# Performance work log

Hardware: AMD Instinct MI355X
Metric: run time of the kernel (lower is better)

## Reference

```python
import jax, jax.numpy as jnp
import numpy as np

N_FZ, N_KEZ, N_TINT, N_ALPHA = 60, 20, 30, 200
NORB, NTIMES = 2000, 1000


def setup_inputs() -> dict:
    key = jax.random.key(0)
    k1, k2, k3, k4 = jax.random.split(key, 4)
    # log-spaced coordinate axes (as built in __init__ from fZs / alphas)
    log_fZs = jnp.linspace(-11.0, -9.0, N_FZ, dtype=jnp.float32)
    log_alphas = jnp.linspace(-2.0, 0.0, N_ALPHA, dtype=jnp.float32)
    alphas = 10.0 ** log_alphas
    kEZs = jnp.linspace(0.5, 10.0, N_KEZ, dtype=jnp.float32)  # sorted for searchsorted
    # grid already in stored layout (n_fZ, n_kEZ, n_tint, n_alpha)
    grid = 20.0 + 5.0 * jax.random.uniform(k1, (N_FZ, N_KEZ, N_TINT, N_ALPHA), dtype=jnp.float32)
    # angular separations, mostly inside [alphas[0], alphas[-1]] with some outside
    alpha = 10.0 ** jax.random.uniform(k2, (NORB, NTIMES), minval=-2.2, maxval=0.1, dtype=jnp.float32)
    dMag = 20.0 + 5.0 * jax.random.uniform(k3, (NORB, NTIMES), dtype=jnp.float32)
    fZ_vals = 10.0 ** jax.random.uniform(k4, (NTIMES,), minval=-11.0, maxval=-9.0, dtype=jnp.float32)
    kEZ_val = jnp.asarray(3.0, dtype=jnp.float32)
    return dict(alpha=alpha, dMag=dMag, fZ_vals=fZ_vals, kEZ_val=kEZ_val,
                grid=grid, kEZs=kEZs, alphas=alphas, log_fZs=log_fZs, log_alphas=log_alphas)


def reference(alpha, dMag, fZ_vals, kEZ_val, grid, kEZs, alphas, log_fZs, log_alphas):
    """Faithful translation of dMag0Grid._pdet_alpha_dMag.

    alpha, dMag : (norb, ntimes); fZ_vals : (ntimes,); kEZ_val : scalar.
    grid : (n_fZ, n_kEZ, n_tint, n_alpha).  Returns pdet : (ntimes, n_tint).
    """
    n_fZ = grid.shape[0]
    n_alpha = grid.shape[-1]
    inv_log_fZ_step = 1.0 / (log_fZs[1] - log_fZs[0])
    inv_log_alpha_step = 1.0 / (log_alphas[1] - log_alphas[0])

    geom_mask = (alpha >= alphas[0]) & (alpha <= alphas[-1])  # (norb, ntimes)

    # log-binned fZ index, per time
    fZ_ind = (jnp.log10(fZ_vals) - log_fZs[0]) * inv_log_fZ_step
    fZ0 = jnp.clip(jnp.floor(fZ_ind).astype(jnp.int32) + 1, 0, n_fZ - 2)  # (ntimes,)

    # log-binned alpha index, per (orbit, time)
    a_ind = (jnp.log10(alpha) - log_alphas[0]) * inv_log_alpha_step
    a0 = jnp.clip(a_ind.astype(jnp.int32), 0, n_alpha - 1)  # (norb, ntimes)
    dalpha = (a_ind - a0).astype(grid.dtype)

    kEZ_ind = jnp.searchsorted(kEZs, kEZ_val, side='right') - 1  # scalar

    # dynamic_slice clamps start so the size-2 window stays in bounds
    a0s = jnp.minimum(a0, n_alpha - 2)
    fZb = jnp.broadcast_to(fZ0[None, :], a0.shape)  # (norb, ntimes)

    sub = grid[:, kEZ_ind]          # (n_fZ, n_tint, n_alpha)
    g0 = sub[fZb, :, a0s]           # (norb, ntimes, n_tint) gather
    g1 = sub[fZb, :, a0s + 1]
    dim = g0 + dalpha[..., None] * (g1 - g0)  # linear interp in log-alpha

    det_mask = geom_mask[..., None] & jnp.signbit(dMag[..., None] - dim)
    pdet = det_mask.mean(axis=0)    # (ntimes, n_tint)
    return pdet
```

## Files before the change

### kernel.cpp

```cpp
#include <hip/hip_runtime.h>
#include <math.h>

#define N_FZ    60
#define N_KEZ   20
#define N_TINT  30
#define N_ALPHA 200
#define NORB    2000
#define NTIMES  1000
#define BLOCK   256

__global__ __launch_bounds__(256) void prep_kernel(
    const float* __restrict__ alpha,
    const float* __restrict__ dMag,
    const float* __restrict__ alphas,
    const float* __restrict__ log_alphas,
    float2* __restrict__ xd)
{
    __shared__ float2 tile[32][33];

    const float la0    = log_alphas[0];
    const float inv_la = 1.0f / (log_alphas[1] - la0);
    const float alo    = alphas[0];
    const float ahi    = alphas[N_ALPHA - 1];

    const int t0 = blockIdx.x * 32;
    const int o0 = blockIdx.y * 32;
    const int tx = threadIdx.x, ty = threadIdx.y;

    #pragma unroll
    for (int r = 0; r < 4; ++r) {
        int orb = o0 + ty + 8 * r;
        int t   = t0 + tx;
        float2 v = make_float2(0.0f, __builtin_inff());
        if (orb < NORB && t < NTIMES) {
            float a  = alpha[(size_t)orb * NTIMES + t];
            float dm = dMag [(size_t)orb * NTIMES + t];
            bool geom = (a >= alo) && (a <= ahi);
            float x = (log10f(a) - la0) * inv_la;
            v = make_float2(x, geom ? dm : __builtin_inff());
        }
        tile[ty + 8 * r][tx] = v;
    }
    __syncthreads();
    #pragma unroll
    for (int r = 0; r < 4; ++r) {
        int tt  = ty + 8 * r;
        int t   = t0 + tt;
        int orb = o0 + tx;
        if (orb < NORB && t < NTIMES)
            xd[(size_t)t * NORB + orb] = tile[tx][tt];
    }
}

__global__ __launch_bounds__(BLOCK) void pdet2_kernel(
    const float2* __restrict__ xd,
    const float* __restrict__ fZ_vals,
    const float* __restrict__ kEZ_val,
    const float* __restrict__ grid,
    const float* __restrict__ kEZs,
    const float* __restrict__ log_fZs,
    float* __restrict__ out)
{
    __shared__ float2 pairs[N_TINT * N_ALPHA];
    __shared__ int    wsum[BLOCK / 64][N_TINT];

    const int t   = blockIdx.x;
    const int tid = threadIdx.x;

    const float lf0    = log_fZs[0];
    const float lfstep = log_fZs[1] - lf0;
    double fZ_ind = (log10((double)fZ_vals[t]) - (double)lf0) * (1.0 / (double)lfstep);
    int fZ0 = (int)floor(fZ_ind) + 1;
    fZ0 = min(max(fZ0, 0), N_FZ - 2);

    const float kv = kEZ_val[0];
    int kidx = -1;
    #pragma unroll
    for (int i = 0; i < N_KEZ; ++i) kidx += (kEZs[i] <= kv) ? 1 : 0;
    if (kidx < 0) kidx += N_KEZ;

    const float* src = grid + ((size_t)fZ0 * N_KEZ + kidx) * (N_TINT * N_ALPHA);
    const float4* src4 = (const float4*)src;
    for (int j = tid; j < (N_TINT * N_ALPHA) / 4; j += BLOCK) {
        float4 v  = src4[j];
        float nxt = src[4 * j + 4];
        pairs[4 * j + 0] = make_float2(v.x, v.y);
        pairs[4 * j + 1] = make_float2(v.y, v.z);
        pairs[4 * j + 2] = make_float2(v.z, v.w);
        pairs[4 * j + 3] = make_float2(v.w, nxt);
    }
    __syncthreads();

    int cnt[N_TINT];
    #pragma unroll
    for (int k = 0; k < N_TINT; ++k) cnt[k] = 0;

    const float4* row = (const float4*)(xd + (size_t)t * NORB);
    for (int i = tid; i < NORB / 2; i += BLOCK) {
        float4 v = row[i];
        float xA = v.x, dmA = v.y;
        float xB = v.z, dmB = v.w;

        int   a0A = min(max((int)xA, 0), N_ALPHA - 1);
        float dalA = xA - (float)a0A;
        int   aA  = min(a0A, N_ALPHA - 2);

        int   a0B = min(max((int)xB, 0), N_ALPHA - 1);
        float dalB = xB - (float)a0B;
        int   aB  = min(a0B, N_ALPHA - 2);

        #pragma unroll
        for (int k = 0; k < N_TINT; ++k) {
            float2 pA = pairs[k * N_ALPHA + aA];
            float2 pB = pairs[k * N_ALPHA + aB];
            float dimA = pA.x + dalA * (pA.y - pA.x);
            float dimB = pB.x + dalB * (pB.y - pB.x);
            cnt[k] += (dmA < dimA) ? 1 : 0;
            cnt[k] += (dmB < dimB) ? 1 : 0;
        }
    }

    const int lane = tid & 63;
    const int wid  = tid >> 6;
    #pragma unroll
    for (int k = 0; k < N_TINT; ++k) {
        int c = cnt[k];
        c += __shfl_xor(c, 32, 64);
        c += __shfl_xor(c, 16, 64);
        c += __shfl_xor(c,  8, 64);
        c += __shfl_xor(c,  4, 64);
        c += __shfl_xor(c,  2, 64);
        c += __shfl_xor(c,  1, 64);
        if (lane == 0) wsum[wid][k] = c;
    }
    __syncthreads();

    if (tid < N_TINT) {
        int tot = wsum[0][tid] + wsum[1][tid] + wsum[2][tid] + wsum[3][tid];
        out[(size_t)t * N_TINT + tid] = (float)tot / (float)NORB;
    }
}

__global__ __launch_bounds__(BLOCK) void pdet_kernel(
    const float* __restrict__ alpha, const float* __restrict__ dMag,
    const float* __restrict__ fZ_vals, const float* __restrict__ kEZ_val,
    const float* __restrict__ grid, const float* __restrict__ kEZs,
    const float* __restrict__ alphas, const float* __restrict__ log_fZs,
    const float* __restrict__ log_alphas, float* __restrict__ out)
{
    __shared__ float2 pairs[N_TINT * N_ALPHA];
    __shared__ int    wsum[BLOCK / 64][N_TINT];

    const int t   = blockIdx.x;
    const int tid = threadIdx.x;

    const float la0    = log_alphas[0];
    const float inv_la = 1.0f / (log_alphas[1] - la0);
    const float alo    = alphas[0];
    const float ahi    = alphas[N_ALPHA - 1];

    const float lf0    = log_fZs[0];
    const float lfstep = log_fZs[1] - lf0;
    double fZ_ind = (log10((double)fZ_vals[t]) - (double)lf0) * (1.0 / (double)lfstep);
    int fZ0 = (int)floor(fZ_ind) + 1;
    fZ0 = min(max(fZ0, 0), N_FZ - 2);

    const float kv = kEZ_val[0];
    int kidx = -1;
    #pragma unroll
    for (int i = 0; i < N_KEZ; ++i) kidx += (kEZs[i] <= kv) ? 1 : 0;
    if (kidx < 0) kidx += N_KEZ;

    const float* src = grid + ((size_t)fZ0 * N_KEZ + kidx) * (N_TINT * N_ALPHA);
    const float4* src4 = (const float4*)src;
    for (int j = tid; j < (N_TINT * N_ALPHA) / 4; j += BLOCK) {
        float4 v  = src4[j];
        float nxt = src[4 * j + 4];
        pairs[4 * j + 0] = make_float2(v.x, v.y);
        pairs[4 * j + 1] = make_float2(v.y, v.z);
        pairs[4 * j + 2] = make_float2(v.z, v.w);
        pairs[4 * j + 3] = make_float2(v.w, nxt);
    }
    __syncthreads();

    int cnt[N_TINT];
    #pragma unroll
    for (int k = 0; k < N_TINT; ++k) cnt[k] = 0;

    for (int orb = tid; orb < NORB; orb += BLOCK) {
        float a  = alpha[(size_t)orb * NTIMES + t];
        float dm = dMag [(size_t)orb * NTIMES + t];
        bool geom = (a >= alo) && (a <= ahi);
        float a_ind = (log10f(a) - la0) * inv_la;
        int a0 = (int)a_ind;
        a0 = min(max(a0, 0), N_ALPHA - 1);
        float dal = a_ind - (float)a0;
        int a0s = min(a0, N_ALPHA - 2);
        if (!geom) dm = __builtin_inff();

        #pragma unroll
        for (int k = 0; k < N_TINT; ++k) {
            float2 p = pairs[k * N_ALPHA + a0s];
            float dim = p.x + dal * (p.y - p.x);
            cnt[k] += (dm < dim) ? 1 : 0;
        }
    }

    const int lane = tid & 63;
    const int wid  = tid >> 6;
    #pragma unroll
    for (int k = 0; k < N_TINT; ++k) {
        int c = cnt[k];
        c += __shfl_xor(c, 32, 64);
        c += __shfl_xor(c, 16, 64);
        c += __shfl_xor(c,  8, 64);
        c += __shfl_xor(c,  4, 64);
        c += __shfl_xor(c,  2, 64);
        c += __shfl_xor(c,  1, 64);
        if (lane == 0) wsum[wid][k] = c;
    }
    __syncthreads();

    if (tid < N_TINT) {
        int tot = wsum[0][tid] + wsum[1][tid] + wsum[2][tid] + wsum[3][tid];
        out[(size_t)t * N_TINT + tid] = (float)tot / (float)NORB;
    }
}

extern "C" void kernel_launch(void* const* d_in, const int* in_sizes, int n_in,
                              void* d_out, int out_size, void* d_ws, size_t ws_size,
                              hipStream_t stream) {
    const float* alpha      = (const float*)d_in[0];
    const float* dMag       = (const float*)d_in[1];
    const float* fZ_vals    = (const float*)d_in[2];
    const float* kEZ_val    = (const float*)d_in[3];
    const float* grid       = (const float*)d_in[4];
    const float* kEZs       = (const float*)d_in[5];
    const float* alphas     = (const float*)d_in[6];
    const float* log_fZs    = (const float*)d_in[7];
    const float* log_alphas = (const float*)d_in[8];
    float* out = (float*)d_out;

    const size_t need = (size_t)NTIMES * NORB * sizeof(float2);
    if (ws_size >= need) {
        dim3 gb((NTIMES + 31) / 32, (NORB + 31) / 32);
        dim3 tb(32, 8);
        prep_kernel<<<gb, tb, 0, stream>>>(alpha, dMag, alphas, log_alphas,
                                           (float2*)d_ws);
        pdet2_kernel<<<NTIMES, BLOCK, 0, stream>>>(
            (const float2*)d_ws, fZ_vals, kEZ_val, grid, kEZs, log_fZs, out);
    } else {
        pdet_kernel<<<NTIMES, BLOCK, 0, stream>>>(
            alpha, dMag, fZ_vals, kEZ_val, grid, kEZs, alphas, log_fZs,
            log_alphas, out);
    }
}
```

Before: 136.5 us.

## Remap threads to tint rows with padded single-float LDS grid

The counting kernel now gives each lane one tint row (k = lane&31) and lets each half-wavefront walk orbits serially, instead of having each thread loop over all 30 tint rows for its own orbits. The grid slice is staged as plain floats with a row stride of 201, so lanes reading the same alpha index from different rows should avoid LDS bank conflicts. This removes the 30-element per-thread counter array and most of the shuffle reduction, which lowers register pressure. In exchange, 2 of every 32 lanes do no useful work, the index math is repeated on every lane, and each thread makes many more serial iterations with broadcast global loads. The alpha index is also clamped before truncation, which changes dalpha slightly at the edges of the range.

```diff
diff --git a/kernel.cpp b/kernel.cpp
--- a/kernel.cpp
+++ b/kernel.cpp
@@ -8,6 +8,7 @@
 #define NORB    2000
 #define NTIMES  1000
 #define BLOCK   256
+#define G_LD    201
 
 __global__ __launch_bounds__(256) void prep_kernel(
     const float* __restrict__ alpha,
@@ -52,7 +53,7 @@
     }
 }
 
-__global__ __launch_bounds__(BLOCK) void pdet2_kernel(
+__global__ __launch_bounds__(BLOCK) void pdet3_kernel(
     const float2* __restrict__ xd,
     const float* __restrict__ fZ_vals,
     const float* __restrict__ kEZ_val,
@@ -61,8 +62,8 @@
     const float* __restrict__ log_fZs,
     float* __restrict__ out)
 {
-    __shared__ float2 pairs[N_TINT * N_ALPHA];
-    __shared__ int    wsum[BLOCK / 64][N_TINT];
+    __shared__ float g[N_TINT * G_LD];
+    __shared__ int   wsum[4][N_TINT];
 
     const int t   = blockIdx.x;
     const int tid = threadIdx.x;
@@ -80,59 +81,46 @@
     if (kidx < 0) kidx += N_KEZ;
 
     const float* src = grid + ((size_t)fZ0 * N_KEZ + kidx) * (N_TINT * N_ALPHA);
-    const float4* src4 = (const float4*)src;
-    for (int j = tid; j < (N_TINT * N_ALPHA) / 4; j += BLOCK) {
-        float4 v  = src4[j];
-        float nxt = src[4 * j + 4];
-        pairs[4 * j + 0] = make_float2(v.x, v.y);
-        pairs[4 * j + 1] = make_float2(v.y, v.z);
-        pairs[4 * j + 2] = make_float2(v.z, v.w);
-        pairs[4 * j + 3] = make_float2(v.w, nxt);
-    }
-    __syncthreads();
-
-    int cnt[N_TINT];
-    #pragma unroll
-    for (int k = 0; k < N_TINT; ++k) cnt[k] = 0;
-
-    const float4* row = (const float4*)(xd + (size_t)t * NORB);
-    for (int i = tid; i < NORB / 2; i += BLOCK) {
-        float4 v = row[i];
-        float xA = v.x, dmA = v.y;
-        float xB = v.z, dmB = v.w;
-
-        int   a0A = min(max((int)xA, 0), N_ALPHA - 1);
-        float dalA = xA - (float)a0A;
-        int   aA  = min(a0A, N_ALPHA - 2);
-
-        int   a0B = min(max((int)xB, 0), N_ALPHA - 1);
-        float dalB = xB - (float)a0B;
-        int   aB  = min(a0B, N_ALPHA - 2);
-
-        #pragma unroll
-        for (int k = 0; k < N_TINT; ++k) {
-            float2 pA = pairs[k * N_ALPHA + aA];
-            float2 pB = pairs[k * N_ALPHA + aB];
-            float dimA = pA.x + dalA * (pA.y - pA.x);
-            float dimB = pB.x + dalB * (pB.y - pB.x);
-            cnt[k] += (dmA < dimA) ? 1 : 0;
-            cnt[k] += (dmB < dimB) ? 1 : 0;
+    for (int m = tid; m < N_TINT * 51; m += BLOCK) {
+        int k = m / 51;
+        int c = m - 51 * k;
+        if (c < 50) {
+            float4 v = *(const float4*)(src + (size_t)k * N_ALPHA + 4 * c);
+            int b = k * G_LD + 4 * c;
+            g[b + 0] = v.x; g[b + 1] = v.y; g[b + 2] = v.z; g[b + 3] = v.w;
+        } else {
+            g[k * G_LD + 200] = src[(size_t)k * N_ALPHA + 200];
         }
     }
+    __syncthreads();
 
     const int lane = tid & 63;
-    const int wid  = tid >> 6;
-    #pragma unroll
-    for (int k = 0; k < N_TINT; ++k) {
-        int c = cnt[k];
-        c += __shfl_xor(c, 32, 64);
-        c += __shfl_xor(c, 16, 64);
-        c += __shfl_xor(c,  8, 64);
-        c += __shfl_xor(c,  4, 64);
-        c += __shfl_xor(c,  2, 64);
-        c += __shfl_xor(c,  1, 64);
-        if (lane == 0) wsum[wid][k] = c;
-    }
+    const int w    = tid >> 6;
+    const int s    = lane >> 5;
+    const int k    = lane & 31;
+    const int krow = min(k, N_TINT - 1) * G_LD;
+    const bool kvalid = (k < N_TINT);
+
+    const float2* row = xd + (size_t)t * NORB;
+    int cnt = 0;
+    #pragma unroll 4
+    for (int i = 0; i < NORB / 8; ++i) {
+        int p = w + 4 * i;
+        float2 v = row[2 * p + s];
+        float x  = v.x;
+        float dm = v.y;
+        float xc = fminf(fmaxf(x, 0.0f), (float)(N_ALPHA - 1));
+        int   a0 = (int)xc;
+        float dal = xc - (float)a0;
+        int   a0s = min(a0, N_ALPHA - 2);
+        float g0 = g[krow + a0s];
+        float g1 = g[krow + a0s + 1];
+        float dim = fmaf(dal, g1 - g0, g0);
+        cnt += (dm < dim) ? 1 : 0;
+    }
+
+    cnt += __shfl_xor(cnt, 32, 64);
+    if (kvalid && s == 0) wsum[w][k] = cnt;
     __syncthreads();
 
     if (tid < N_TINT) {
@@ -247,7 +235,7 @@
         dim3 tb(32, 8);
         prep_kernel<<<gb, tb, 0, stream>>>(alpha, dMag, alphas, log_alphas,
                                            (float2*)d_ws);
-        pdet2_kernel<<<NTIMES, BLOCK, 0, stream>>>(
+        pdet3_kernel<<<NTIMES, BLOCK, 0, stream>>>(
             (const float2*)d_ws, fZ_vals, kEZ_val, grid, kEZs, log_fZs, out);
     } else {
         pdet_kernel<<<NTIMES, BLOCK, 0, stream>>>(
```

After: 139.8 us. +2.5%, slower.
